# Optimization experiments

Measured on AMD Instinct MI355X. Metric: run time of the kernel, lower is better.

## Reference

```python
import jax, jax.numpy as jnp
import numpy as np

EPS = 1e-5


def _gcn_norm(edge_index, N):
    # symmetric GCN normalization with self-loops: D^-1/2 (A+I) D^-1/2
    row, col = edge_index[0], edge_index[1]
    loop = jnp.arange(N, dtype=row.dtype)
    row_f = jnp.concatenate([row, loop])
    col_f = jnp.concatenate([col, loop])
    deg = jax.ops.segment_sum(jnp.ones_like(row_f, dtype=jnp.float32), row_f, num_segments=N)
    dinv = jnp.where(deg > 0, jax.lax.rsqrt(jnp.maximum(deg, 1.0)), 0.0)
    norm = dinv[row_f] * dinv[col_f]  # [E+N]
    return row_f, col_f, norm


def _gcn_conv(h, W, b, row_f, col_f, norm, N):
    h = h @ W  # [N, C_out] small GEMM
    msg = h[col_f] * norm[:, None]  # gather over edges  [E+N, C_out]
    return jax.ops.segment_sum(msg, row_f, num_segments=N) + b


def _bn_eval(h, gamma, beta, mean, var):
    return (h - mean) * jax.lax.rsqrt(var + EPS) * gamma + beta


def setup_inputs() -> dict:
    key = jax.random.key(0)
    ks = jax.random.split(key, 12)
    N, E = 100000, 1600000
    C_in, C_hid, C_out = 64, 64, 64
    x = jax.random.normal(ks[0], (N, C_in), dtype=jnp.float32)
    edge_index = jax.random.randint(ks[1], (2, E), 0, N, dtype=jnp.int32)
    s = 1.0 / np.sqrt(C_hid)
    inp = {
        "x": x,
        "edge_index": edge_index,
        "W1": jax.random.normal(ks[2], (C_in, C_hid), dtype=jnp.float32) * s,
        "b1": jnp.zeros((C_hid,), jnp.float32),
        "g1": jnp.ones((C_hid,), jnp.float32),
        "be1": jnp.zeros((C_hid,), jnp.float32),
        "m1": jax.random.normal(ks[3], (C_hid,), dtype=jnp.float32) * 0.1,
        "v1": jax.random.uniform(ks[4], (C_hid,), minval=0.5, maxval=1.5, dtype=jnp.float32),
        "W2": jax.random.normal(ks[5], (C_hid, C_hid), dtype=jnp.float32) * s,
        "b2": jnp.zeros((C_hid,), jnp.float32),
        "g2": jnp.ones((C_hid,), jnp.float32),
        "be2": jnp.zeros((C_hid,), jnp.float32),
        "m2": jax.random.normal(ks[6], (C_hid,), dtype=jnp.float32) * 0.1,
        "v2": jax.random.uniform(ks[7], (C_hid,), minval=0.5, maxval=1.5, dtype=jnp.float32),
        "W3": jax.random.normal(ks[8], (C_hid, C_out), dtype=jnp.float32) * s,
        "b3": jnp.zeros((C_out,), jnp.float32),
    }
    return inp


def reference(x, edge_index, W1, b1, g1, be1, m1, v1, W2, b2, g2, be2, m2, v2, W3, b3):
    N = x.shape[0]
    row_f, col_f, norm = _gcn_norm(edge_index, N)  # cached=True: computed once
    h = _gcn_conv(x, W1, b1, row_f, col_f, norm, N)
    h = jax.nn.relu(_bn_eval(h, g1, be1, m1, v1))  # dropout off (eval)
    h = _gcn_conv(h, W2, b2, row_f, col_f, norm, N)
    h = jax.nn.relu(_bn_eval(h, g2, be2, m2, v2))
    global_embeddings = h
    hc_predictions = _gcn_conv(global_embeddings, W3, b3, row_f, col_f, norm, N)
    return (global_embeddings, hc_predictions)
```

## Files before the change

kernel.cpp:

```cpp
#include <hip/hip_runtime.h>

typedef __attribute__((ext_vector_type(8))) short bfrag8;
typedef __attribute__((ext_vector_type(4))) float facc4;
typedef __attribute__((ext_vector_type(8))) unsigned short u16x8;

#define CROWS  256
#define NCBMAX 512
#define CAP    8192
#define CHUNK  4096
#define SLACK  772

static __device__ __forceinline__ float bf2f(ushort u) {
    union { unsigned int i; float f; } x;
    x.i = ((unsigned int)u) << 16;
    return x.f;
}
static __device__ __forceinline__ ushort f2bf(float f) {
    union { float f; unsigned int i; } x;
    x.f = f;
    unsigned int r = x.i + 0x7FFFu + ((x.i >> 16) & 1u);
    return (ushort)(r >> 16);
}


__global__ void k_cinit(int* __restrict__ ccur, int ncb, ushort* __restrict__ t, int N) {
    int b = blockIdx.x * blockDim.x + threadIdx.x;
    if (b < ncb) ccur[b] = b * CAP;
    if (blockIdx.x == 0 && threadIdx.x < 64) t[(size_t)N * 64 + threadIdx.x] = 0;
}

__global__ void k_part(const int* __restrict__ row, const int* __restrict__ col, int E,
                       int* __restrict__ ccur, int* __restrict__ bkt, int ncb) {
    __shared__ int recs[CHUNK];
    __shared__ unsigned short cbl[CHUNK];
    __shared__ int hist[NCBMAX], lbase[NCBMAX], loff[NCBMAX];
    int tid = threadIdx.x;
    int chunk0 = blockIdx.x * CHUNK;
    for (int i = tid; i < ncb; i += blockDim.x) hist[i] = 0;
    __syncthreads();
    for (int j = tid; j < CHUNK; j += blockDim.x) {
        int e = chunk0 + j;
        if (e < E) {
            int r = row[e];
            int cb = r >> 8;
            recs[j] = ((r & (CROWS - 1)) << 17) | col[e];
            cbl[j] = (unsigned short)cb;
            atomicAdd(&hist[cb], 1);
        } else cbl[j] = 0xFFFF;
    }
    __syncthreads();
    for (int i = tid; i < ncb; i += blockDim.x) {
        int h = hist[i];
        lbase[i] = h ? atomicAdd(&ccur[i], h) : 0;
        loff[i] = 0;
    }
    __syncthreads();
    for (int j = tid; j < CHUNK; j += blockDim.x) {
        unsigned short cb = cbl[j];
        if (cb != 0xFFFF) {
            int p = lbase[cb] + atomicAdd(&loff[cb], 1);
            if (p < (cb + 1) * CAP) bkt[p] = recs[j];
        }
    }
}

__global__ void k_scan(const int* __restrict__ ccur, int* __restrict__ cbase, int ncb) {
    __shared__ int tmp[NCBMAX];
    int tid = threadIdx.x;
    int v = (tid < ncb) ? min(ccur[tid] - tid * CAP, CAP) : 0;
    tmp[tid] = v;
    __syncthreads();
    #pragma unroll
    for (int off = 1; off < NCBMAX; off <<= 1) {
        int t = (tid >= off) ? tmp[tid - off] : 0;
        __syncthreads();
        tmp[tid] += t;
        __syncthreads();
    }
    if (tid < ncb) cbase[tid] = tmp[tid] - v;
    if (tid == ncb - 1) cbase[ncb] = tmp[tid];
}

__global__ void k_build(const int* __restrict__ bkt, const int* __restrict__ ccur,
                        const int* __restrict__ cbase,
                        int* __restrict__ rptr, int* __restrict__ deg,
                        float* __restrict__ dinv, int* __restrict__ cidx, int N) {
    __shared__ int hist[CROWS], wstart[CROWS], cur[CROWS], psum[CROWS];
    int tid = threadIdx.x;
    int b = blockIdx.x;
    int lo = b * CROWS;
    int nr = min(CROWS, N - lo);
    int in0 = b * CAP;
    int cntE = min(ccur[b] - in0, CAP);
    int out0 = ((cbase[b] + 3) & ~3) + b * SLACK;

    hist[tid] = 0;
    __syncthreads();
    for (int i = tid; i < cntE; i += blockDim.x)
        atomicAdd(&hist[bkt[in0 + i] >> 17], 1);
    __syncthreads();
    int d = hist[tid];
    int ep = (d + 3) & ~3;
    psum[tid] = ep;
    __syncthreads();
    #pragma unroll
    for (int off = 1; off < CROWS; off <<= 1) {
        int t = (tid >= off) ? psum[tid - off] : 0;
        __syncthreads();
        psum[tid] += t;
        __syncthreads();
    }
    int ws = out0 + psum[tid] - ep;
    wstart[tid] = ws;
    cur[tid] = ws;
    if (tid < nr) {
        rptr[lo + tid] = ws;
        deg[lo + tid] = d;
        dinv[lo + tid] = rsqrtf((float)(d + 1));
    }
    __syncthreads();
    for (int i = tid; i < cntE; i += blockDim.x) {
        int v = bkt[in0 + i];
        int p = atomicAdd(&cur[v >> 17], 1);
        cidx[p] = v & 0x1FFFF;
    }
    __syncthreads();
    if (tid < nr)
        for (int j = d; j < ep; j++) cidx[wstart[tid] + j] = N;
}

template <bool FP32IN>
__global__ void k_gemm(const void* __restrict__ Hv, const float* __restrict__ W,
                       const float* __restrict__ dinv,
                       ushort* __restrict__ T, int ntiles, int N) {
    int lane = threadIdx.x & 63;
    int wid = (blockIdx.x * blockDim.x + threadIdx.x) >> 6;
    int nw = (gridDim.x * blockDim.x) >> 6;
    int m = lane & 15, quad = lane >> 4;

    bfrag8 bf[2][4];
    #pragma unroll
    for (int s = 0; s < 2; s++)
        #pragma unroll
        for (int c = 0; c < 4; c++) {
            bfrag8 f;
            #pragma unroll
            for (int j = 0; j < 8; j++) {
                int k = 32 * s + quad * 8 + j;
                f[j] = (short)f2bf(W[k * 64 + 16 * c + m]);
            }
            bf[s][c] = f;
        }

    for (int t = wid; t < ntiles; t += nw) {
        int nodeA = t * 16 + m;
        if (nodeA >= N) nodeA = N - 1;
        bfrag8 a0, a1;
        if (FP32IN) {
            const float* arow = (const float*)Hv + (size_t)nodeA * 64;
            #pragma unroll
            for (int s = 0; s < 2; s++) {
                float4 u0 = *(const float4*)(arow + s * 32 + quad * 8);
                float4 u1 = *(const float4*)(arow + s * 32 + quad * 8 + 4);
                bfrag8 f;
                f[0] = (short)f2bf(u0.x); f[1] = (short)f2bf(u0.y);
                f[2] = (short)f2bf(u0.z); f[3] = (short)f2bf(u0.w);
                f[4] = (short)f2bf(u1.x); f[5] = (short)f2bf(u1.y);
                f[6] = (short)f2bf(u1.z); f[7] = (short)f2bf(u1.w);
                if (s == 0) a0 = f; else a1 = f;
            }
        } else {
            const ushort* arow = (const ushort*)Hv + (size_t)nodeA * 64;
            a0 = *(const bfrag8*)(arow + quad * 8);
            a1 = *(const bfrag8*)(arow + 32 + quad * 8);
        }
        facc4 acc[4];
        #pragma unroll
        for (int c = 0; c < 4; c++) { acc[c][0]=0.f; acc[c][1]=0.f; acc[c][2]=0.f; acc[c][3]=0.f; }
        #pragma unroll
        for (int c = 0; c < 4; c++) {
            acc[c] = __builtin_amdgcn_mfma_f32_16x16x32_bf16(a0, bf[0][c], acc[c], 0, 0, 0);
            acc[c] = __builtin_amdgcn_mfma_f32_16x16x32_bf16(a1, bf[1][c], acc[c], 0, 0, 0);
        }
        #pragma unroll
        for (int c = 0; c < 4; c++)
            #pragma unroll
            for (int r = 0; r < 4; r++) {
                int node = t * 16 + quad * 4 + r;
                if (node < N)
                    T[(size_t)node * 64 + c * 16 + m] = f2bf(dinv[node] * acc[c][r]);
            }
    }
}

__global__ void k_agg(const ushort* __restrict__ T2, const int* __restrict__ rptr,
                      const int* __restrict__ deg, const float* __restrict__ dinv,
                      const int* __restrict__ cidx,
                      const float* __restrict__ bias, const float* __restrict__ g,
                      const float* __restrict__ be, const float* __restrict__ mm,
                      const float* __restrict__ vv, int do_bn,
                      float* __restrict__ outf, ushort* __restrict__ outb, int N) {
    int lane = threadIdx.x & 63;
    int wid = (blockIdx.x * blockDim.x + threadIdx.x) >> 6;
    int nw = (gridDim.x * blockDim.x) >> 6;
    int grp = lane >> 3;
    int s = lane & 7;

    float bb[8], sc[8], sh[8];
    #pragma unroll
    for (int k = 0; k < 8; k++) { bb[k] = bias[s * 8 + k]; sc[k] = 1.f; sh[k] = 0.f; }
    if (do_bn) {
        #pragma unroll
        for (int k = 0; k < 8; k++) {
            sc[k] = g[s * 8 + k] * rsqrtf(vv[s * 8 + k] + 1e-5f);
            sh[k] = be[s * 8 + k] - mm[s * 8 + k] * sc[k];
        }
    }

    int noct = (N + 7) >> 3;
    for (int q = wid; q < noct; q += nw) {
        int r = q * 8 + grp;
        bool rv = (r < N);
        int start = rv ? rptr[r] : 0;
        int ep = rv ? ((deg[r] + 3) & ~3) : 0;
        float a[8];
        #pragma unroll
        for (int k = 0; k < 8; k++) a[k] = 0.f;
        for (int i = 0; i < ep; i += 4) {
            int4 c4 = *(const int4*)(cidx + start + i);
            u16x8 t0 = *(const u16x8*)(T2 + (size_t)c4.x * 64 + s * 8);
            u16x8 t1 = *(const u16x8*)(T2 + (size_t)c4.y * 64 + s * 8);
            u16x8 t2 = *(const u16x8*)(T2 + (size_t)c4.z * 64 + s * 8);
            u16x8 t3 = *(const u16x8*)(T2 + (size_t)c4.w * 64 + s * 8);
            #pragma unroll
            for (int k = 0; k < 8; k++)
                a[k] += (bf2f(t0[k]) + bf2f(t1[k])) + (bf2f(t2[k]) + bf2f(t3[k]));
        }
        if (rv) {
            u16x8 sf = *(const u16x8*)(T2 + (size_t)r * 64 + s * 8);
            float dr = dinv[r];
            float v[8];
            #pragma unroll
            for (int k = 0; k < 8; k++) {
                v[k] = dr * (a[k] + bf2f(sf[k])) + bb[k];
                if (do_bn) v[k] = fmaxf(v[k] * sc[k] + sh[k], 0.f);
            }
            if (outf) {
                *(float4*)(outf + (size_t)r * 64 + s * 8) = make_float4(v[0], v[1], v[2], v[3]);
                *(float4*)(outf + (size_t)r * 64 + s * 8 + 4) = make_float4(v[4], v[5], v[6], v[7]);
            }
            if (outb) {
                u16x8 o;
                #pragma unroll
                for (int k = 0; k < 8; k++) o[k] = f2bf(v[k]);
                *(u16x8*)(outb + (size_t)r * 64 + s * 8) = o;
            }
        }
    }
}


extern "C" void kernel_launch(void* const* d_in, const int* in_sizes, int n_in,
                              void* d_out, int out_size, void* d_ws, size_t ws_size,
                              hipStream_t stream) {
    const float* x  = (const float*)d_in[0];
    const int*   ei = (const int*)d_in[1];
    const float *W1 = (const float*)d_in[2],  *b1 = (const float*)d_in[3];
    const float *g1 = (const float*)d_in[4],  *be1= (const float*)d_in[5];
    const float *m1 = (const float*)d_in[6],  *v1 = (const float*)d_in[7];
    const float *W2 = (const float*)d_in[8],  *b2 = (const float*)d_in[9];
    const float *g2 = (const float*)d_in[10], *be2= (const float*)d_in[11];
    const float *m2 = (const float*)d_in[12], *v2 = (const float*)d_in[13];
    const float *W3 = (const float*)d_in[14], *b3 = (const float*)d_in[15];

    int N = in_sizes[0] / 64;
    int E = in_sizes[1] / 2;
    const int* row = ei;
    const int* col = ei + E;
    int ncb = (N + CROWS - 1) / CROWS;

    char* p = (char*)d_ws;
    auto take = [&](size_t b) -> char* {
        char* q = p;
        p += (b + 255) & ~(size_t)255;
        return q;
    };
    int*    ccur  = (int*)   take((size_t)ncb * 4);
    int*    cbase = (int*)   take((size_t)(ncb + 1) * 4);
    int*    rptr  = (int*)   take((size_t)N * 4);
    int*    deg   = (int*)   take((size_t)N * 4);
    float*  dinv  = (float*) take((size_t)N * 4);
    int*    bkt   = (int*)   take((size_t)ncb * CAP * 4);
    int*    cidx  = (int*)   take((size_t)(E + ncb * SLACK + 64) * 4);
    ushort* t     = (ushort*)take((size_t)(N + 1) * 64 * 2);
    ushort* h     = (ushort*)take((size_t)N * 64 * 2);

    const int TB = 256;
    int nchunks = (E + CHUNK - 1) / CHUNK;
    k_cinit<<<(ncb + TB - 1) / TB, TB, 0, stream>>>(ccur, ncb, t, N);
    k_part <<<nchunks, TB, 0, stream>>>(row, col, E, ccur, bkt, ncb);
    k_scan <<<1, NCBMAX, 0, stream>>>(ccur, cbase, ncb);
    k_build<<<ncb, TB, 0, stream>>>(bkt, ccur, cbase, rptr, deg, dinv, cidx, N);

    float* outp = (float*)d_out;
    int ntiles = (N + 15) >> 4;
    const int GG = 1024;
    int noct = (N + 7) >> 3;
    int GA = (noct + 3) / 4;

    k_gemm<true> <<<GG, TB, 0, stream>>>(x, W1, dinv, t, ntiles, N);
    k_agg <<<GA, TB, 0, stream>>>(t, rptr, deg, dinv, cidx, b1, g1, be1, m1, v1, 1,
                                  (float*)nullptr, h, N);
    k_gemm<false><<<GG, TB, 0, stream>>>(h, W2, dinv, t, ntiles, N);
    k_agg <<<GA, TB, 0, stream>>>(t, rptr, deg, dinv, cidx, b2, g2, be2, m2, v2, 1,
                                  outp, h, N);
    k_gemm<false><<<GG, TB, 0, stream>>>(h, W3, dinv, t, ntiles, N);
    k_agg <<<GA, TB, 0, stream>>>(t, rptr, deg, dinv, cidx, b3, b3, b3, b3, b3, 0,
                                  outp + (size_t)N * 64, (ushort*)nullptr, N);
}
```

Baseline: 292.6 us.

## Drop global scan kernel with fixed-pitch CSR buckets; enlarge partition/build blocks

Removes the single-block k_scan launch by giving each coarse bucket a fixed output region of CAP+SLACK entries in the column-index array, so k_build no longer needs a global prefix sum. The partition and build kernels now run with 1024 threads per block, and k_build guards its per-row shared-memory work to the first 256 threads. The GEMM grid is sized from the tile count instead of a fixed 1024 blocks. The change saves a launch and a serialization point at the cost of a larger, sparser cidx layout with padding gaps between buckets.

```diff
diff --git a/kernel.cpp b/kernel.cpp
--- a/kernel.cpp
+++ b/kernel.cpp
@@ -9,6 +9,7 @@
 #define CAP    8192
 #define CHUNK  4096
 #define SLACK  772
+#define BPITCH (CAP + SLACK)
 
 static __device__ __forceinline__ float bf2f(ushort u) {
     union { unsigned int i; float f; } x;
@@ -64,25 +65,7 @@
     }
 }
 
-__global__ void k_scan(const int* __restrict__ ccur, int* __restrict__ cbase, int ncb) {
-    __shared__ int tmp[NCBMAX];
-    int tid = threadIdx.x;
-    int v = (tid < ncb) ? min(ccur[tid] - tid * CAP, CAP) : 0;
-    tmp[tid] = v;
-    __syncthreads();
-    #pragma unroll
-    for (int off = 1; off < NCBMAX; off <<= 1) {
-        int t = (tid >= off) ? tmp[tid - off] : 0;
-        __syncthreads();
-        tmp[tid] += t;
-        __syncthreads();
-    }
-    if (tid < ncb) cbase[tid] = tmp[tid] - v;
-    if (tid == ncb - 1) cbase[ncb] = tmp[tid];
-}
-
 __global__ void k_build(const int* __restrict__ bkt, const int* __restrict__ ccur,
-                        const int* __restrict__ cbase,
                         int* __restrict__ rptr, int* __restrict__ deg,
                         float* __restrict__ dinv, int* __restrict__ cidx, int N) {
     __shared__ int hist[CROWS], wstart[CROWS], cur[CROWS], psum[CROWS];
@@ -92,31 +75,36 @@
     int nr = min(CROWS, N - lo);
     int in0 = b * CAP;
     int cntE = min(ccur[b] - in0, CAP);
-    int out0 = ((cbase[b] + 3) & ~3) + b * SLACK;
-
-    hist[tid] = 0;
+    int out0 = b * BPITCH;
+
+    if (tid < CROWS) hist[tid] = 0;
     __syncthreads();
     for (int i = tid; i < cntE; i += blockDim.x)
         atomicAdd(&hist[bkt[in0 + i] >> 17], 1);
     __syncthreads();
-    int d = hist[tid];
-    int ep = (d + 3) & ~3;
-    psum[tid] = ep;
+    int d = 0, ep = 0;
+    if (tid < CROWS) {
+        d = hist[tid];
+        ep = (d + 3) & ~3;
+        psum[tid] = ep;
+    }
     __syncthreads();
     #pragma unroll
     for (int off = 1; off < CROWS; off <<= 1) {
-        int t = (tid >= off) ? psum[tid - off] : 0;
+        int t = (tid >= off && tid < CROWS) ? psum[tid - off] : 0;
         __syncthreads();
-        psum[tid] += t;
+        if (tid < CROWS) psum[tid] += t;
         __syncthreads();
     }
-    int ws = out0 + psum[tid] - ep;
-    wstart[tid] = ws;
-    cur[tid] = ws;
-    if (tid < nr) {
-        rptr[lo + tid] = ws;
-        deg[lo + tid] = d;
-        dinv[lo + tid] = rsqrtf((float)(d + 1));
+    if (tid < CROWS) {
+        int ws = out0 + psum[tid] - ep;
+        wstart[tid] = ws;
+        cur[tid] = ws;
+        if (tid < nr) {
+            rptr[lo + tid] = ws;
+            deg[lo + tid] = d;
+            dinv[lo + tid] = rsqrtf((float)(d + 1));
+        }
     }
     __syncthreads();
     for (int i = tid; i < cntE; i += blockDim.x) {
@@ -286,25 +274,24 @@
         return q;
     };
     int*    ccur  = (int*)   take((size_t)ncb * 4);
-    int*    cbase = (int*)   take((size_t)(ncb + 1) * 4);
     int*    rptr  = (int*)   take((size_t)N * 4);
     int*    deg   = (int*)   take((size_t)N * 4);
     float*  dinv  = (float*) take((size_t)N * 4);
     int*    bkt   = (int*)   take((size_t)ncb * CAP * 4);
-    int*    cidx  = (int*)   take((size_t)(E + ncb * SLACK + 64) * 4);
+    int*    cidx  = (int*)   take((size_t)ncb * BPITCH * 4 + 1024);
     ushort* t     = (ushort*)take((size_t)(N + 1) * 64 * 2);
     ushort* h     = (ushort*)take((size_t)N * 64 * 2);
 
     const int TB = 256;
+    const int TBP = 1024;
     int nchunks = (E + CHUNK - 1) / CHUNK;
     k_cinit<<<(ncb + TB - 1) / TB, TB, 0, stream>>>(ccur, ncb, t, N);
-    k_part <<<nchunks, TB, 0, stream>>>(row, col, E, ccur, bkt, ncb);
-    k_scan <<<1, NCBMAX, 0, stream>>>(ccur, cbase, ncb);
-    k_build<<<ncb, TB, 0, stream>>>(bkt, ccur, cbase, rptr, deg, dinv, cidx, N);
+    k_part <<<nchunks, TBP, 0, stream>>>(row, col, E, ccur, bkt, ncb);
+    k_build<<<ncb, TBP, 0, stream>>>(bkt, ccur, rptr, deg, dinv, cidx, N);
 
     float* outp = (float*)d_out;
     int ntiles = (N + 15) >> 4;
-    const int GG = 1024;
+    int GG = (ntiles + 3) / 4;
     int noct = (N + 7) >> 3;
     int GA = (noct + 3) / 4;
 
```

New measurement: 283.0 us. 1.03x faster.
